# Performance work log

Measured on AMD Instinct MI355X. Metric: run time of the kernel, lower is better.

The kernel has to match this reference:

```python
import jax, jax.numpy as jnp
import numpy as np

N, D, L, K = 32, 128, 3136, 64

def setup_inputs() -> dict:
    key = jax.random.key(0)
    k1, k2, k3 = jax.random.split(key, 3)
    x = jax.random.normal(k1, (N, D, L), dtype=jnp.float32)
    weight = jax.random.normal(k2, (K, D), dtype=jnp.float32)  # codebook centers
    scale = jax.random.normal(k3, (1,), dtype=jnp.float32)
    return {"x": x, "weight": weight, "scale": scale}

def reference(x, weight, scale):
    # x: (N, C, ...) -> (N, D, L); output scaled squared L2 dist (N, K, L)
    n, c = x.shape[0], x.shape[1]
    xf = x.reshape(n, c, -1)  # (N, D, L)
    x_sq = jnp.sum(xf * xf, axis=1)          # (N, L)
    c_sq = jnp.sum(weight * weight, axis=1)  # (K,)
    xc = jnp.einsum('ndl,kd->nkl', xf, weight)  # (N, K, L)
    dist = x_sq[:, None, :] + c_sq[None, :, None] - 2.0 * xc
    return dist / (scale[0] ** 2)
```

## Files before the change

kernel.cpp:

```cpp
#include <hip/hip_runtime.h>

#define N_ 32
#define D_ 128
#define L_ 3136
#define K_ 64

typedef short bf16x8 __attribute__((ext_vector_type(8)));
typedef float f32x4  __attribute__((ext_vector_type(4)));

__device__ inline unsigned short f2bf(float f) {
    unsigned u = __float_as_uint(f);
    return (unsigned short)((u + 0x7FFFu + ((u >> 16) & 1u)) >> 16);
}
__device__ inline float bf2f(unsigned short h) {
    return __uint_as_float(((unsigned)h) << 16);
}

__global__ __launch_bounds__(64) void prep_kernel(
    const float* __restrict__ w,
    unsigned short* __restrict__ whi,
    unsigned short* __restrict__ wlo,
    float* __restrict__ csq)
{
    const int b = blockIdx.x, lane = threadIdx.x;
    if (b < 16) {
        const int dc = b >> 2, kt = b & 3;
        const int row = kt * 16 + (lane & 15);
        const int d0  = dc * 32 + (lane >> 4) * 8;
        const float* src = w + row * D_ + d0;
        __attribute__((aligned(16))) unsigned short h[8], l[8];
#pragma unroll
        for (int j = 0; j < 8; ++j) {
            float v = src[j];
            h[j] = f2bf(v);
            l[j] = f2bf(v - bf2f(h[j]));
        }
        const size_t off = (size_t)(b * 64 + lane) * 8;
        *(ushort4*)(whi + off)     = *(const ushort4*)(h);
        *(ushort4*)(whi + off + 4) = *(const ushort4*)(h + 4);
        *(ushort4*)(wlo + off)     = *(const ushort4*)(l);
        *(ushort4*)(wlo + off + 4) = *(const ushort4*)(l + 4);
    } else {
        const float* wr = w + lane * D_;
        float s = 0.f;
#pragma unroll
        for (int d = 0; d < D_; d += 4) {
            float4 v = *(const float4*)(wr + d);
            s = fmaf(v.x, v.x, s); s = fmaf(v.y, v.y, s);
            s = fmaf(v.z, v.z, s); s = fmaf(v.w, v.w, s);
        }
        csq[lane] = s;
    }
}

__global__ __launch_bounds__(256, 4) void enc_mfma_kernel(
    const float* __restrict__ x,
    const unsigned short* __restrict__ whi,
    const unsigned short* __restrict__ wlo,
    const float* __restrict__ csqg,
    const float* __restrict__ scale,
    float* __restrict__ out)
{
    __shared__ __attribute__((aligned(16))) unsigned short lds_w[2 * 8192];
    __shared__ float lds_csq[K_];
    __shared__ float lds_xsq[64];
    float* lds_c = (float*)lds_w;

    const int t    = threadIdx.x;
    const int wave = t >> 6;
    const int lane = t & 63;
    const int col  = lane & 15;
    const int quad = lane >> 4;
    const int n    = blockIdx.y;
    const int l0   = blockIdx.x * 64;

#pragma unroll
    for (int i = 0; i < 8; ++i) {
        const int c = wave * 8 + i;
        const unsigned short* g =
            (c < 16 ? whi + (size_t)c * 512 : wlo + (size_t)(c - 16) * 512) + lane * 8;
        __builtin_amdgcn_global_load_lds(
            (const __attribute__((address_space(1))) unsigned int*)g,
            (__attribute__((address_space(3))) unsigned int*)&lds_w[c * 512],
            16, 0, 0);
    }
    if (wave == 0) {
        __builtin_amdgcn_global_load_lds(
            (const __attribute__((address_space(1))) unsigned int*)(csqg + lane),
            (__attribute__((address_space(3))) unsigned int*)lds_csq,
            4, 0, 0);
    }
    __syncthreads();

    const float* xa = x + (size_t)n * D_ * L_ + l0 + wave * 16 + col;

    f32x4 acc[4];
#pragma unroll
    for (int kt = 0; kt < 4; ++kt) acc[kt] = (f32x4){0.f, 0.f, 0.f, 0.f};
    float xsq = 0.f;

#pragma unroll
    for (int dc = 0; dc < 4; ++dc) {
        const float* xp = xa + (size_t)(dc * 32 + quad * 8) * L_;
        float xv[8];
#pragma unroll
        for (int j = 0; j < 8; ++j) xv[j] = xp[(size_t)j * L_];

        __attribute__((aligned(16))) unsigned short ah[8], al[8];
#pragma unroll
        for (int j = 0; j < 8; ++j) {
            xsq = fmaf(xv[j], xv[j], xsq);
            unsigned short h = f2bf(xv[j]);
            ah[j] = h;
            al[j] = f2bf(xv[j] - bf2f(h));
        }
        bf16x8 afh = *(const bf16x8*)ah;
        bf16x8 afl = *(const bf16x8*)al;

#pragma unroll
        for (int kt = 0; kt < 4; ++kt) {
            const int fo = ((dc * 4 + kt) * 64 + lane) * 8;
            bf16x8 bh = *(const bf16x8*)&lds_w[fo];
            bf16x8 bl = *(const bf16x8*)&lds_w[8192 + fo];
            acc[kt] = __builtin_amdgcn_mfma_f32_16x16x32_bf16(afh, bh, acc[kt], 0, 0, 0);
            acc[kt] = __builtin_amdgcn_mfma_f32_16x16x32_bf16(afl, bh, acc[kt], 0, 0, 0);
            acc[kt] = __builtin_amdgcn_mfma_f32_16x16x32_bf16(afh, bl, acc[kt], 0, 0, 0);
        }
    }

    xsq += __shfl_xor(xsq, 16, 64);
    xsq += __shfl_xor(xsq, 32, 64);
    if (quad == 0) lds_xsq[wave * 16 + col] = xsq;

    __syncthreads();

#pragma unroll
    for (int kt = 0; kt < 4; ++kt) {
        const int kk = kt * 16 + col;
#pragma unroll
        for (int r = 0; r < 4; ++r) {
            const int ll = wave * 16 + quad * 4 + r;
            lds_c[kk * 65 + ll] = acc[kt][r];
        }
    }
    __syncthreads();

    const float sc = scale[0];
    const float inv_s2 = 1.0f / (sc * sc);
    float* op = out + (size_t)n * K_ * L_ + l0;
#pragma unroll
    for (int it = 0; it < 16; ++it) {
        const int idx = it * 256 + t;
        const int kk = idx >> 6, ll = idx & 63;
        op[(size_t)kk * L_ + ll] =
            (lds_xsq[ll] + lds_csq[kk] - 2.0f * lds_c[kk * 65 + ll]) * inv_s2;
    }
}

extern "C" void kernel_launch(void* const* d_in, const int* in_sizes, int n_in,
                              void* d_out, int out_size, void* d_ws, size_t ws_size,
                              hipStream_t stream) {
    const float* x     = (const float*)d_in[0];
    const float* w     = (const float*)d_in[1];
    const float* scale = (const float*)d_in[2];
    float* out = (float*)d_out;

    unsigned short* whi = (unsigned short*)d_ws;
    unsigned short* wlo = (unsigned short*)((char*)d_ws + 16384);
    float*          csq = (float*)((char*)d_ws + 32768);

    prep_kernel<<<17, 64, 0, stream>>>(w, whi, wlo, csq);
    dim3 grid(L_ / 64, N_);
    enc_mfma_kernel<<<grid, 256, 0, stream>>>(x, whi, wlo, csq, scale, out);
}
```

Measured before the change: 101.0 us.

## Replace split-bf16 triple MFMA with single fp16 MFMA and direct register epilogue

```diff
diff --git a/kernel.cpp b/kernel.cpp
--- a/kernel.cpp
+++ b/kernel.cpp
@@ -5,21 +5,12 @@
 #define L_ 3136
 #define K_ 64
 
-typedef short bf16x8 __attribute__((ext_vector_type(8)));
-typedef float f32x4  __attribute__((ext_vector_type(4)));
-
-__device__ inline unsigned short f2bf(float f) {
-    unsigned u = __float_as_uint(f);
-    return (unsigned short)((u + 0x7FFFu + ((u >> 16) & 1u)) >> 16);
-}
-__device__ inline float bf2f(unsigned short h) {
-    return __uint_as_float(((unsigned)h) << 16);
-}
+typedef _Float16 f16x8 __attribute__((ext_vector_type(8)));
+typedef float    f32x4 __attribute__((ext_vector_type(4)));
 
 __global__ __launch_bounds__(64) void prep_kernel(
     const float* __restrict__ w,
-    unsigned short* __restrict__ whi,
-    unsigned short* __restrict__ wlo,
+    unsigned short* __restrict__ wh,
     float* __restrict__ csq)
 {
     const int b = blockIdx.x, lane = threadIdx.x;
@@ -28,18 +19,15 @@
         const int row = kt * 16 + (lane & 15);
         const int d0  = dc * 32 + (lane >> 4) * 8;
         const float* src = w + row * D_ + d0;
-        __attribute__((aligned(16))) unsigned short h[8], l[8];
+        __attribute__((aligned(16))) unsigned short h[8];
 #pragma unroll
         for (int j = 0; j < 8; ++j) {
-            float v = src[j];
-            h[j] = f2bf(v);
-            l[j] = f2bf(v - bf2f(h[j]));
+            _Float16 v = (_Float16)src[j];
+            h[j] = *(const unsigned short*)&v;
         }
         const size_t off = (size_t)(b * 64 + lane) * 8;
-        *(ushort4*)(whi + off)     = *(const ushort4*)(h);
-        *(ushort4*)(whi + off + 4) = *(const ushort4*)(h + 4);
-        *(ushort4*)(wlo + off)     = *(const ushort4*)(l);
-        *(ushort4*)(wlo + off + 4) = *(const ushort4*)(l + 4);
+        *(ushort4*)(wh + off)     = *(const ushort4*)(h);
+        *(ushort4*)(wh + off + 4) = *(const ushort4*)(h + 4);
     } else {
         const float* wr = w + lane * D_;
         float s = 0.f;
@@ -53,18 +41,15 @@
     }
 }
 
-__global__ __launch_bounds__(256, 4) void enc_mfma_kernel(
+__global__ __launch_bounds__(256, 6) void enc_mfma_kernel(
     const float* __restrict__ x,
-    const unsigned short* __restrict__ whi,
-    const unsigned short* __restrict__ wlo,
+    const unsigned short* __restrict__ wh,
     const float* __restrict__ csqg,
     const float* __restrict__ scale,
     float* __restrict__ out)
 {
-    __shared__ __attribute__((aligned(16))) unsigned short lds_w[2 * 8192];
+    __shared__ __attribute__((aligned(16))) unsigned short lds_w[8192];
     __shared__ float lds_csq[K_];
-    __shared__ float lds_xsq[64];
-    float* lds_c = (float*)lds_w;
 
     const int t    = threadIdx.x;
     const int wave = t >> 6;
@@ -75,12 +60,10 @@
     const int l0   = blockIdx.x * 64;
 
 #pragma unroll
-    for (int i = 0; i < 8; ++i) {
-        const int c = wave * 8 + i;
-        const unsigned short* g =
-            (c < 16 ? whi + (size_t)c * 512 : wlo + (size_t)(c - 16) * 512) + lane * 8;
+    for (int i = 0; i < 4; ++i) {
+        const int c = wave * 4 + i;
         __builtin_amdgcn_global_load_lds(
-            (const __attribute__((address_space(1))) unsigned int*)g,
+            (const __attribute__((address_space(1))) unsigned int*)(wh + (size_t)c * 512 + lane * 8),
             (__attribute__((address_space(3))) unsigned int*)&lds_w[c * 512],
             16, 0, 0);
     }
@@ -106,54 +89,40 @@
 #pragma unroll
         for (int j = 0; j < 8; ++j) xv[j] = xp[(size_t)j * L_];
 
-        __attribute__((aligned(16))) unsigned short ah[8], al[8];
+        union { f16x8 v; _Float16 e[8]; } af;
 #pragma unroll
         for (int j = 0; j < 8; ++j) {
             xsq = fmaf(xv[j], xv[j], xsq);
-            unsigned short h = f2bf(xv[j]);
-            ah[j] = h;
-            al[j] = f2bf(xv[j] - bf2f(h));
+            af.e[j] = (_Float16)xv[j];
         }
-        bf16x8 afh = *(const bf16x8*)ah;
-        bf16x8 afl = *(const bf16x8*)al;
 
 #pragma unroll
         for (int kt = 0; kt < 4; ++kt) {
             const int fo = ((dc * 4 + kt) * 64 + lane) * 8;
-            bf16x8 bh = *(const bf16x8*)&lds_w[fo];
-            bf16x8 bl = *(const bf16x8*)&lds_w[8192 + fo];
-            acc[kt] = __builtin_amdgcn_mfma_f32_16x16x32_bf16(afh, bh, acc[kt], 0, 0, 0);
-            acc[kt] = __builtin_amdgcn_mfma_f32_16x16x32_bf16(afl, bh, acc[kt], 0, 0, 0);
-            acc[kt] = __builtin_amdgcn_mfma_f32_16x16x32_bf16(afh, bl, acc[kt], 0, 0, 0);
+            f16x8 bf = *(const f16x8*)&lds_w[fo];
+            acc[kt] = __builtin_amdgcn_mfma_f32_16x16x32_f16(af.v, bf, acc[kt], 0, 0, 0);
         }
     }
 
     xsq += __shfl_xor(xsq, 16, 64);
     xsq += __shfl_xor(xsq, 32, 64);
-    if (quad == 0) lds_xsq[wave * 16 + col] = xsq;
-
-    __syncthreads();
-
+    float xs[4];
 #pragma unroll
-    for (int kt = 0; kt < 4; ++kt) {
-        const int kk = kt * 16 + col;
-#pragma unroll
-        for (int r = 0; r < 4; ++r) {
-            const int ll = wave * 16 + quad * 4 + r;
-            lds_c[kk * 65 + ll] = acc[kt][r];
-        }
-    }
-    __syncthreads();
+    for (int r = 0; r < 4; ++r)
+        xs[r] = __shfl(xsq, quad * 4 + r, 64);
 
     const float sc = scale[0];
     const float inv_s2 = 1.0f / (sc * sc);
-    float* op = out + (size_t)n * K_ * L_ + l0;
+    float* op = out + (size_t)n * K_ * L_ + l0 + wave * 16 + quad * 4;
 #pragma unroll
-    for (int it = 0; it < 16; ++it) {
-        const int idx = it * 256 + t;
-        const int kk = idx >> 6, ll = idx & 63;
-        op[(size_t)kk * L_ + ll] =
-            (lds_xsq[ll] + lds_csq[kk] - 2.0f * lds_c[kk * 65 + ll]) * inv_s2;
+    for (int kt = 0; kt < 4; ++kt) {
+        const float cs = lds_csq[kt * 16 + col];
+        float4 v;
+        v.x = (xs[0] + cs - 2.0f * acc[kt][0]) * inv_s2;
+        v.y = (xs[1] + cs - 2.0f * acc[kt][1]) * inv_s2;
+        v.z = (xs[2] + cs - 2.0f * acc[kt][2]) * inv_s2;
+        v.w = (xs[3] + cs - 2.0f * acc[kt][3]) * inv_s2;
+        *(float4*)(op + (size_t)(kt * 16 + col) * L_) = v;
     }
 }
 
@@ -165,11 +134,10 @@
     const float* scale = (const float*)d_in[2];
     float* out = (float*)d_out;
 
-    unsigned short* whi = (unsigned short*)d_ws;
-    unsigned short* wlo = (unsigned short*)((char*)d_ws + 16384);
-    float*          csq = (float*)((char*)d_ws + 32768);
+    unsigned short* wh  = (unsigned short*)d_ws;
+    float*          csq = (float*)((char*)d_ws + 16384);
 
-    prep_kernel<<<17, 64, 0, stream>>>(w, whi, wlo, csq);
+    prep_kernel<<<17, 64, 0, stream>>>(w, wh, csq);
     dim3 grid(L_ / 64, N_);
-    enc_mfma_kernel<<<grid, 256, 0, stream>>>(x, whi, wlo, csq, scale, out);
+    enc_mfma_kernel<<<grid, 256, 0, stream>>>(x, wh, csq, scale, out);
 }
```

Measured after the change: 97.88 us. 1.03x faster.
